# Kernel tuning notes

Measured on AMD Instinct MI355X. Metric: run time of the kernel, lower is better.

Reference implementation:

```python
import jax, jax.numpy as jnp
import numpy as np

DIM = 128    # dim (LSTM hidden size)
P = 8        # pooling_size (maxout pool width)
K = 2        # number of experts
STEPS = 4    # max_decoding_steps
M = 4096     # document length


def setup_inputs() -> dict:
    d, p, k, m = DIM, P, K, M
    keys = jax.random.split(jax.random.key(0), 26)
    s = 0.05

    def rn(kk, shape):
        return jax.random.normal(kk, shape, jnp.float32) * s

    inp = {"U": jax.random.normal(keys[0], (1, m, 2 * d), jnp.float32)}
    inp["lstm_Wih"] = rn(keys[1], (4 * d, 4 * d))
    inp["lstm_Whh"] = rn(keys[2], (4 * d, d))
    inp["lstm_bih"] = rn(keys[3], (4 * d,))
    inp["lstm_bhh"] = rn(keys[4], (4 * d,))
    i = 5
    for suf in ("s", "e"):
        inp[f"Wr_{suf}"] = rn(keys[i], (d, 5 * d)); i += 1
        inp[f"br_{suf}"] = rn(keys[i], (d,)); i += 1
        inp[f"Wg_{suf}"] = rn(keys[i], (k, 5 * d)); i += 1
        inp[f"bg_{suf}"] = rn(keys[i], (k,)); i += 1
        inp[f"We_{suf}"] = rn(keys[i], (k, p * d, 3 * d)); i += 1
        inp[f"be_{suf}"] = rn(keys[i], (k, p * d)); i += 1
        inp[f"W2_{suf}"] = rn(keys[i], (p * d, d)); i += 1
        inp[f"b2_{suf}"] = rn(keys[i], (p * d,)); i += 1
        inp[f"W3_{suf}"] = rn(keys[i], (p, 2 * d)); i += 1
        inp[f"b3_{suf}"] = rn(keys[i], (p,)); i += 1
    return inp


def _forward(U, lstm_Wih, lstm_Whh, lstm_bih, lstm_bhh,
             Wr_s, br_s, Wg_s, bg_s, We_s, be_s, W2_s, b2_s, W3_s, b3_s,
             Wr_e, br_e, Wg_e, bg_e, We_e, be_e, W2_e, b2_e, W3_e, b3_e):
    d, p = DIM, P
    Useq = U[0]                      # (m, 2d)
    m = Useq.shape[0]

    def lstm_step(x, h, c):
        g = lstm_Wih @ x + lstm_Whh @ h + lstm_bih + lstm_bhh
        i, f, gg, o = jnp.split(g, 4)  # torch LSTM gate order: i, f, g, o
        c2 = jax.nn.sigmoid(f) * c + jax.nn.sigmoid(i) * jnp.tanh(gg)
        return jax.nn.sigmoid(o) * jnp.tanh(c2), c2

    def experts(h, us, ue, Wr, br, Wg, bg, We, be):
        ctx = jnp.concatenate([h, us, ue])                 # (5d,)
        r = jnp.tanh(Wr @ ctx + br)                        # (d,)
        gate = jax.nn.softmax(Wg @ ctx + bg)               # (k,)
        inp = jnp.concatenate([Useq, jnp.broadcast_to(r, (m, d))], axis=-1)  # (m, 3d)
        z = jnp.einsum('mf,kef->kme', inp, We) + be[:, None, :]              # (k, m, p*d)
        z = z.reshape(K, m, p, d).max(axis=2)              # maxout -> (k, m, d)
        return jnp.einsum('k,kmd->md', gate, z)            # mixture -> (m, d)

    def hmn(m1, W2, b2, W3, b3):
        m2 = (m1 @ W2.T + b2).reshape(m, p, d).max(axis=1)                    # (m, d)
        return (jnp.concatenate([m1, m2], axis=-1) @ W3.T + b3).max(axis=-1)  # (m,)

    h = jnp.zeros((d,), U.dtype)
    c = jnp.zeros((d,), U.dtype)
    si = jnp.array(0, jnp.int32)
    ei = jnp.array(m - 1, jnp.int32)
    starts, ends = [], []
    for _ in range(STEPS):
        us = jnp.take(Useq, si, axis=0)
        ue = jnp.take(Useq, ei, axis=0)
        h, c = lstm_step(jnp.concatenate([us, ue]), h, c)
        ls = hmn(experts(h, us, ue, Wr_s, br_s, Wg_s, bg_s, We_s, be_s), W2_s, b2_s, W3_s, b3_s)
        le = hmn(experts(h, us, ue, Wr_e, br_e, Wg_e, bg_e, We_e, be_e), W2_e, b2_e, W3_e, b3_e)
        si = jnp.argmax(ls).astype(jnp.int32)
        ei = jnp.argmax(le).astype(jnp.int32)
        starts.append(ls)
        ends.append(le)
    # torch.cat of (1,1,m) along dim=-2 -> (1, STEPS, m)
    return jnp.stack(starts)[None], jnp.stack(ends)[None]


def reference(U, lstm_Wih, lstm_Whh, lstm_bih, lstm_bhh,
              Wr_s, br_s, Wg_s, bg_s, We_s, be_s, W2_s, b2_s, W3_s, b3_s,
              Wr_e, br_e, Wg_e, bg_e, We_e, be_e, W2_e, b2_e, W3_e, b3_e):
    return _forward(U, lstm_Wih, lstm_Whh, lstm_bih, lstm_bhh,
                    Wr_s, br_s, Wg_s, bg_s, We_s, be_s, W2_s, b2_s, W3_s, b3_s,
                    Wr_e, br_e, Wg_e, bg_e, We_e, be_e, W2_e, b2_e, W3_e, b3_e)
```

## Files before the change

### kernel.cpp

```cpp
#include <hip/hip_runtime.h>
#include <math.h>

#define DD   128
#define MM   4096
#define NSTEP 4
#define NEG_INF (-3.4e38f)

#define WS_H0   0
#define WS_C0   256
#define WS_G    512
#define WS_RS   1024
#define WS_RE   1152
#define WS_GS   1280
#define WS_SIEI 1284
#define WS_RT   2048
#define WS_Z0   8192
#define WS_W2S  (8192 + 16777216)
#define WS_USP  (WS_W2S + 262144)
#define WS_WESP (WS_USP + 1048576)
#define WS_END2 (WS_W2S + 262144)
#define WS_END4 (WS_WESP + 1048576)
#define W2SPLIT_N 262144
#define USPLIT_N  1048576
#define WESPLIT_N 1048576

typedef __attribute__((ext_vector_type(8))) short bf16x8;
typedef __attribute__((ext_vector_type(4))) float f32x4;
typedef __attribute__((ext_vector_type(4))) unsigned short u16x4;

static __device__ __forceinline__ unsigned short f2b(float x) {
  unsigned u = __float_as_uint(x);
  unsigned r = (u + 0x7fffu + ((u >> 16) & 1u)) >> 16;
  return (unsigned short)r;
}
static __device__ __forceinline__ float b2f(unsigned short h) {
  return __uint_as_float(((unsigned)h) << 16);
}
static __device__ __forceinline__ void split4(float4 v, u16x4* h, u16x4* l) {
  unsigned short h0 = f2b(v.x), h1 = f2b(v.y), h2 = f2b(v.z), h3 = f2b(v.w);
  u16x4 hh = {h0, h1, h2, h3};
  u16x4 ll = {f2b(v.x - b2f(h0)), f2b(v.y - b2f(h1)),
              f2b(v.z - b2f(h2)), f2b(v.w - b2f(h3))};
  *h = hh; *l = ll;
}
static __device__ __forceinline__ float sigm(float x) {
  return 1.f / (1.f + expf(-x));
}

__global__ void k_init(float* __restrict__ ws) {
  int t = threadIdx.x;
  if (t < 128) { ws[WS_H0 + t] = 0.f; ws[WS_C0 + t] = 0.f; }
}

__global__ void k_prep(const float* __restrict__ W2_s,
                       const float* __restrict__ W2_e,
                       const float* __restrict__ U,
                       const float* __restrict__ We_s, const float* __restrict__ We_e,
                       int do4, float* __restrict__ ws) {
  unsigned short* w2h = (unsigned short*)(ws + WS_W2S);
  unsigned short* w2l = w2h + W2SPLIT_N;
  unsigned short* uh = (unsigned short*)(ws + WS_USP);
  unsigned short* ul = uh + USPLIT_N;
  unsigned short* wh = (unsigned short*)(ws + WS_WESP);
  unsigned short* wl = wh + WESPLIT_N;
  int total = do4 ? (W2SPLIT_N + USPLIT_N + WESPLIT_N) : W2SPLIT_N;
  for (int i = blockIdx.x * blockDim.x + threadIdx.x; i < total;
       i += gridDim.x * blockDim.x) {
    if (i < W2SPLIT_N) {
      int suf = i >> 17;
      int rem = i & 131071;
      float v = (suf ? W2_e : W2_s)[rem];
      unsigned short h = f2b(v);
      w2h[i] = h; w2l[i] = f2b(v - b2f(h));
    } else if (i < W2SPLIT_N + USPLIT_N) {
      int j = i - W2SPLIT_N;
      float v = U[j];
      unsigned short h = f2b(v);
      uh[j] = h; ul[j] = f2b(v - b2f(h));
    } else {
      int j = i - W2SPLIT_N - USPLIT_N;
      int z = j >> 18;
      int rem = j & 262143;
      int e = rem >> 8, f = rem & 255;
      int suf = z >> 1, k = z & 1;
      const float* We = suf ? We_e : We_s;
      float v = We[((size_t)k * 1024 + e) * 384 + f];
      unsigned short h = f2b(v);
      wh[j] = h; wl[j] = f2b(v - b2f(h));
    }
  }
}

__global__ __launch_bounds__(256) void k_z0m2(float* __restrict__ ws) {
  __shared__ unsigned short Ah[128][40];
  __shared__ unsigned short Al[128][40];
  __shared__ unsigned short Bh[128][40];
  __shared__ unsigned short Bl[128][40];
  float* z0 = ws + WS_Z0;
  const unsigned short* uh = (const unsigned short*)(ws + WS_USP);
  const unsigned short* ul = uh + USPLIT_N;
  const unsigned short* wh = (const unsigned short*)(ws + WS_WESP);
  const unsigned short* wl = wh + WESPLIT_N;

  int t = threadIdx.x;
  int lane = t & 63, wid = t >> 6;
  int wm = wid >> 1, wn = wid & 1;
  int lr = lane & 15, lk = (lane >> 4) * 8, lq = lane >> 4;
  int m0 = blockIdx.x * 128, e0 = blockIdx.y * 128;
  int z = blockIdx.z;
  const unsigned short* bh0 = wh + (size_t)z * 262144;
  const unsigned short* bl0 = wl + (size_t)z * 262144;

  f32x4 acc[4][4];
  f32x4 zz = {0.f, 0.f, 0.f, 0.f};
#pragma unroll
  for (int i = 0; i < 4; ++i)
#pragma unroll
    for (int n = 0; n < 4; ++n) acc[i][n] = zz;

  for (int kc = 0; kc < 8; ++kc) {
    int k0 = kc * 32;
    __syncthreads();
#pragma unroll
    for (int it = 0; it < 2; ++it) {
      int idx = t + it * 256;
      int row = idx >> 2, q8 = (idx & 3) * 8;
      size_t goff = (size_t)(m0 + row) * 256 + k0 + q8;
      *(uint4*)&Ah[row][q8] = *(const uint4*)&uh[goff];
      *(uint4*)&Al[row][q8] = *(const uint4*)&ul[goff];
      size_t boff = (size_t)(e0 + row) * 256 + k0 + q8;
      *(uint4*)&Bh[row][q8] = *(const uint4*)&bh0[boff];
      *(uint4*)&Bl[row][q8] = *(const uint4*)&bl0[boff];
    }
    __syncthreads();
    bf16x8 ah[4], al[4], bh[4], bl[4];
#pragma unroll
    for (int i = 0; i < 4; ++i) {
      ah[i] = *(bf16x8*)&Ah[wm * 64 + i * 16 + lr][lk];
      al[i] = *(bf16x8*)&Al[wm * 64 + i * 16 + lr][lk];
    }
#pragma unroll
    for (int n = 0; n < 4; ++n) {
      bh[n] = *(bf16x8*)&Bh[wn * 64 + n * 16 + lr][lk];
      bl[n] = *(bf16x8*)&Bl[wn * 64 + n * 16 + lr][lk];
    }
#pragma unroll
    for (int i = 0; i < 4; ++i)
#pragma unroll
      for (int n = 0; n < 4; ++n) {
        acc[i][n] = __builtin_amdgcn_mfma_f32_16x16x32_bf16(ah[i], bh[n], acc[i][n], 0, 0, 0);
        acc[i][n] = __builtin_amdgcn_mfma_f32_16x16x32_bf16(ah[i], bl[n], acc[i][n], 0, 0, 0);
        acc[i][n] = __builtin_amdgcn_mfma_f32_16x16x32_bf16(al[i], bh[n], acc[i][n], 0, 0, 0);
      }
  }

  float* C = z0 + (size_t)z * MM * 1024;
#pragma unroll
  for (int i = 0; i < 4; ++i)
#pragma unroll
    for (int n = 0; n < 4; ++n)
#pragma unroll
      for (int r = 0; r < 4; ++r) {
        int row = m0 + wm * 64 + i * 16 + lq * 4 + r;
        int col = e0 + wn * 64 + n * 16 + lr;
        C[(size_t)row * 1024 + col] = acc[i][n][r];
      }
}

__global__ __launch_bounds__(256) void k_z0m(
    const float* __restrict__ U,
    const float* __restrict__ We_s, const float* __restrict__ We_e,
    float* __restrict__ ws) {
  __shared__ unsigned short Ah[128][40];
  __shared__ unsigned short Al[128][40];
  __shared__ unsigned short Bh[128][40];
  __shared__ unsigned short Bl[128][40];
  float* z0 = ws + WS_Z0;

  int t = threadIdx.x;
  int lane = t & 63, wid = t >> 6;
  int wm = wid >> 1, wn = wid & 1;
  int lr = lane & 15, lk = (lane >> 4) * 8, lq = lane >> 4;
  int m0 = blockIdx.x * 128, e0 = blockIdx.y * 128;
  int z = blockIdx.z;
  int suf = z >> 1, k = z & 1;
  const float* Wep = (suf ? We_e : We_s) + (size_t)k * 1024 * 384;

  f32x4 acc[4][4];
  f32x4 zz = {0.f, 0.f, 0.f, 0.f};
#pragma unroll
  for (int i = 0; i < 4; ++i)
#pragma unroll
    for (int n = 0; n < 4; ++n) acc[i][n] = zz;

  for (int kc = 0; kc < 8; ++kc) {
    int k0 = kc * 32;
    __syncthreads();
#pragma unroll
    for (int it = 0; it < 4; ++it) {
      int idx = t + it * 256;
      int row = idx >> 3, q = idx & 7;
      float4 va = *(const float4*)&U[(size_t)(m0 + row) * 256 + k0 + q * 4];
      u16x4 h, l; split4(va, &h, &l);
      *(u16x4*)&Ah[row][q * 4] = h;
      *(u16x4*)&Al[row][q * 4] = l;
      float4 vb = *(const float4*)&Wep[(size_t)(e0 + row) * 384 + k0 + q * 4];
      split4(vb, &h, &l);
      *(u16x4*)&Bh[row][q * 4] = h;
      *(u16x4*)&Bl[row][q * 4] = l;
    }
    __syncthreads();
    bf16x8 ah[4], al[4], bh[4], bl[4];
#pragma unroll
    for (int i = 0; i < 4; ++i) {
      ah[i] = *(bf16x8*)&Ah[wm * 64 + i * 16 + lr][lk];
      al[i] = *(bf16x8*)&Al[wm * 64 + i * 16 + lr][lk];
    }
#pragma unroll
    for (int n = 0; n < 4; ++n) {
      bh[n] = *(bf16x8*)&Bh[wn * 64 + n * 16 + lr][lk];
      bl[n] = *(bf16x8*)&Bl[wn * 64 + n * 16 + lr][lk];
    }
#pragma unroll
    for (int i = 0; i < 4; ++i)
#pragma unroll
      for (int n = 0; n < 4; ++n) {
        acc[i][n] = __builtin_amdgcn_mfma_f32_16x16x32_bf16(ah[i], bh[n], acc[i][n], 0, 0, 0);
        acc[i][n] = __builtin_amdgcn_mfma_f32_16x16x32_bf16(ah[i], bl[n], acc[i][n], 0, 0, 0);
        acc[i][n] = __builtin_amdgcn_mfma_f32_16x16x32_bf16(al[i], bh[n], acc[i][n], 0, 0, 0);
      }
  }

  float* C = z0 + (size_t)z * MM * 1024;
#pragma unroll
  for (int i = 0; i < 4; ++i)
#pragma unroll
    for (int n = 0; n < 4; ++n)
#pragma unroll
      for (int r = 0; r < 4; ++r) {
        int row = m0 + wm * 64 + i * 16 + lq * 4 + r;
        int col = e0 + wn * 64 + n * 16 + lr;
        C[(size_t)row * 1024 + col] = acc[i][n][r];
      }
}

__global__ __launch_bounds__(256) void k_gates(
    const float* __restrict__ U,
    const float* __restrict__ Wih, const float* __restrict__ Whh,
    const float* __restrict__ bih, const float* __restrict__ bhh,
    const float* __restrict__ out, int step,
    float* __restrict__ ws) {
  __shared__ float ctx2[640];
  __shared__ float rv[256];
  __shared__ int   ri[256];
  __shared__ int   sei[2];
  int t = threadIdx.x;
  int b = blockIdx.x;

  if (step > 0) {
    int half = t >> 7, l = t & 127;
    const float* arr = out + (size_t)half * (NSTEP * MM) + (size_t)(step - 1) * MM;
    float bv = NEG_INF; int bi = 0;
    for (int i = l; i < MM; i += 128) {
      float v = arr[i];
      if (v > bv) { bv = v; bi = i; }
    }
    rv[t] = bv; ri[t] = bi;
    __syncthreads();
    for (int s = 64; s > 0; s >>= 1) {
      if (l < s) {
        float v2 = rv[t + s]; int i2 = ri[t + s];
        if (v2 > rv[t] || (v2 == rv[t] && i2 < ri[t])) { rv[t] = v2; ri[t] = i2; }
      }
      __syncthreads();
    }
    if (l == 0) sei[half] = ri[t];
    __syncthreads();
  } else {
    if (t == 0) { sei[0] = 0; sei[1] = MM - 1; }
    __syncthreads();
  }
  int si = sei[0], ei = sei[1];
  if (b == 0 && t == 0) { ((int*)ws)[WS_SIEI] = si; ((int*)ws)[WS_SIEI + 1] = ei; }

  ctx2[t]       = U[(size_t)si * 256 + t];
  ctx2[256 + t] = U[(size_t)ei * 256 + t];
  if (t < 128) ctx2[512 + t] = ws[WS_H0 + (step & 1) * 128 + t];
  __syncthreads();

  int row = b * 16 + (t >> 4), sub = t & 15;
  const float* wih = Wih + (size_t)row * 512;
  const float* whh = Whh + (size_t)row * 128;
  float acc = 0.f;
  int e0 = sub * 40;
#pragma unroll
  for (int e = e0; e < e0 + 40; e += 4) {
    float4 w = (e < 512) ? *(const float4*)&wih[e] : *(const float4*)&whh[e - 512];
    acc += w.x * ctx2[e] + w.y * ctx2[e + 1] + w.z * ctx2[e + 2] + w.w * ctx2[e + 3];
  }
#pragma unroll
  for (int off = 8; off > 0; off >>= 1) acc += __shfl_down(acc, off, 16);
  if (sub == 0) ws[WS_G + row] = acc + bih[row] + bhh[row];
}

__global__ __launch_bounds__(256) void k_r(
    const float* __restrict__ U,
    const float* __restrict__ Wr_s, const float* __restrict__ br_s,
    const float* __restrict__ Wg_s, const float* __restrict__ bg_s,
    const float* __restrict__ Wr_e, const float* __restrict__ br_e,
    const float* __restrict__ Wg_e, const float* __restrict__ bg_e,
    int step, float* __restrict__ ws) {
  __shared__ float ctxR[640];
  __shared__ float gl[512];
  __shared__ float logit[4];
  int t = threadIdx.x, b = blockIdx.x;
  int si = ((const int*)ws)[WS_SIEI], ei = ((const int*)ws)[WS_SIEI + 1];

  gl[t] = ws[WS_G + t];
  gl[256 + t] = ws[WS_G + 256 + t];
  ctxR[128 + t] = U[(size_t)si * 256 + t];
  ctxR[384 + t] = U[(size_t)ei * 256 + t];
  __syncthreads();
  if (t < 128) {
    float ig = sigm(gl[t]);
    float fg = sigm(gl[128 + t]);
    float gg = tanhf(gl[256 + t]);
    float og = sigm(gl[384 + t]);
    float cp = ws[WS_C0 + (step & 1) * 128 + t];
    float c2 = fg * cp + ig * gg;
    float h2 = og * tanhf(c2);
    ctxR[t] = h2;
    if (b == 16) {
      ws[WS_C0 + ((step + 1) & 1) * 128 + t] = c2;
      ws[WS_H0 + ((step + 1) & 1) * 128 + t] = h2;
    }
  }
  __syncthreads();

  if (b < 16) {
    int rr = b * 16 + (t >> 4), sub = t & 15;
    int suf = rr >> 7, i = rr & 127;
    const float* Wr = suf ? Wr_e : Wr_s;
    const float* br = suf ? br_e : br_s;
    const float* w = Wr + (size_t)i * 640;
    float acc = 0.f;
    int e0 = sub * 40;
#pragma unroll
    for (int e = e0; e < e0 + 40; e += 4) {
      float4 wv = *(const float4*)&w[e];
      acc += wv.x * ctxR[e] + wv.y * ctxR[e + 1] + wv.z * ctxR[e + 2] + wv.w * ctxR[e + 3];
    }
#pragma unroll
    for (int off = 8; off > 0; off >>= 1) acc += __shfl_down(acc, off, 16);
    if (sub == 0) ws[(suf ? WS_RE : WS_RS) + i] = tanhf(acc + br[i]);
  } else {
    if (t < 64) {
      int which = t >> 4, sub = t & 15;
      const float* Wg = (which < 2) ? Wg_s : Wg_e;
      const float* bg = (which < 2) ? bg_s : bg_e;
      int i = which & 1;
      const float* w = Wg + (size_t)i * 640;
      float acc = 0.f;
      int e0 = sub * 40;
#pragma unroll
      for (int e = e0; e < e0 + 40; e += 4) {
        float4 wv = *(const float4*)&w[e];
        acc += wv.x * ctxR[e] + wv.y * ctxR[e + 1] + wv.z * ctxR[e + 2] + wv.w * ctxR[e + 3];
      }
#pragma unroll
      for (int off = 8; off > 0; off >>= 1) acc += __shfl_down(acc, off, 16);
      if (sub == 0) logit[which] = acc + bg[i];
    }
    __syncthreads();
    if (t == 0) {
      float a = logit[0], bb = logit[1], mx = fmaxf(a, bb);
      float ea = expf(a - mx), eb = expf(bb - mx), s = ea + eb;
      ws[WS_GS + 0] = ea / s; ws[WS_GS + 1] = eb / s;
      a = logit[2]; bb = logit[3]; mx = fmaxf(a, bb);
      ea = expf(a - mx); eb = expf(bb - mx); s = ea + eb;
      ws[WS_GS + 2] = ea / s; ws[WS_GS + 3] = eb / s;
    }
  }
}

__global__ __launch_bounds__(256) void k_rt(
    const float* __restrict__ We_s, const float* __restrict__ be_s,
    const float* __restrict__ We_e, const float* __restrict__ be_e,
    float* __restrict__ ws) {
  __shared__ float rsh[256];
  int t = threadIdx.x, b = blockIdx.x;
  rsh[t] = ws[WS_RS + t];
  __syncthreads();
  int lrw = t >> 2, sub = t & 3;
  int row = b * 64 + lrw;
  int suf = row >> 11, ke = row & 2047;
  const float* We = suf ? We_e : We_s;
  const float* be = suf ? be_e : be_s;
  const float* w = We + (size_t)ke * 384 + 256;
  const float* r = rsh + suf * 128;
  float acc = 0.f;
  int e0 = sub * 32;
#pragma unroll
  for (int e = e0; e < e0 + 32; e += 4) {
    float4 wv = *(const float4*)&w[e];
    acc += wv.x * r[e] + wv.y * r[e + 1] + wv.z * r[e + 2] + wv.w * r[e + 3];
  }
#pragma unroll
  for (int off = 2; off > 0; off >>= 1) acc += __shfl_down(acc, off, 4);
  if (sub == 0) ws[WS_RT + row] = acc + be[ke];
}

__global__ __launch_bounds__(256) void k_score3(
    const float* __restrict__ b2_a, const float* __restrict__ W3_a, const float* __restrict__ b3_a,
    const float* __restrict__ b2_b, const float* __restrict__ W3_b, const float* __restrict__ b3_b,
    float* __restrict__ out_a, float* __restrict__ out_b,
    float* __restrict__ ws) {
  __shared__ float rtm[2048];
  __shared__ float m1f[16][132];
  __shared__ float m2f[16][132];
  __shared__ float sj[16][8];

  const float* z0 = ws + WS_Z0;
  const unsigned short* w2base = (const unsigned short*)(ws + WS_W2S);

  int t = threadIdx.x;
  int suf = blockIdx.y;
  int m0 = blockIdx.x * 16;
  const float* b2 = suf ? b2_b : b2_a;
  const float* W3 = suf ? W3_b : W3_a;
  const float* b3 = suf ? b3_b : b3_a;
  float*     outp = suf ? out_b : out_a;
  const unsigned short* w2h = w2base + (size_t)suf * 131072;
  const unsigned short* w2l = w2base + W2SPLIT_N + (size_t)suf * 131072;

  for (int l = t; l < 2048; l += 256) rtm[l] = ws[WS_RT + suf * 2048 + l];
  float g0 = ws[WS_GS + suf * 2 + 0];
  float g1 = ws[WS_GS + suf * 2 + 1];
  __syncthreads();

  {
    int row = t >> 4, c8 = (t & 15) * 8;
    const float* p0 = z0 + ((size_t)(suf * 2 + 0) * MM + m0 + row) * 1024 + c8;
    const float* p1 = z0 + ((size_t)(suf * 2 + 1) * MM + m0 + row) * 1024 + c8;
    float4 mxa0 = {NEG_INF, NEG_INF, NEG_INF, NEG_INF}, mxb0 = mxa0;
    float4 mxa1 = mxa0, mxb1 = mxa0;
#pragma unroll
    for (int pp = 0; pp < 8; ++pp) {
      float4 va0 = *(const float4*)&p0[pp * 128];
      float4 vb0 = *(const float4*)&p0[pp * 128 + 4];
      float4 ra0 = *(const float4*)&rtm[pp * 128 + c8];
      float4 rb0 = *(const float4*)&rtm[pp * 128 + c8 + 4];
      mxa0.x = fmaxf(mxa0.x, va0.x + ra0.x); mxa0.y = fmaxf(mxa0.y, va0.y + ra0.y);
      mxa0.z = fmaxf(mxa0.z, va0.z + ra0.z); mxa0.w = fmaxf(mxa0.w, va0.w + ra0.w);
      mxb0.x = fmaxf(mxb0.x, vb0.x + rb0.x); mxb0.y = fmaxf(mxb0.y, vb0.y + rb0.y);
      mxb0.z = fmaxf(mxb0.z, vb0.z + rb0.z); mxb0.w = fmaxf(mxb0.w, vb0.w + rb0.w);
      float4 va1 = *(const float4*)&p1[pp * 128];
      float4 vb1 = *(const float4*)&p1[pp * 128 + 4];
      float4 ra1 = *(const float4*)&rtm[1024 + pp * 128 + c8];
      float4 rb1 = *(const float4*)&rtm[1024 + pp * 128 + c8 + 4];
      mxa1.x = fmaxf(mxa1.x, va1.x + ra1.x); mxa1.y = fmaxf(mxa1.y, va1.y + ra1.y);
      mxa1.z = fmaxf(mxa1.z, va1.z + ra1.z); mxa1.w = fmaxf(mxa1.w, va1.w + ra1.w);
      mxb1.x = fmaxf(mxb1.x, vb1.x + rb1.x); mxb1.y = fmaxf(mxb1.y, vb1.y + rb1.y);
      mxb1.z = fmaxf(mxb1.z, vb1.z + rb1.z); mxb1.w = fmaxf(mxb1.w, vb1.w + rb1.w);
    }
    float4 o0 = {g0 * mxa0.x + g1 * mxa1.x, g0 * mxa0.y + g1 * mxa1.y,
                 g0 * mxa0.z + g1 * mxa1.z, g0 * mxa0.w + g1 * mxa1.w};
    float4 o1 = {g0 * mxb0.x + g1 * mxb1.x, g0 * mxb0.y + g1 * mxb1.y,
                 g0 * mxb0.z + g1 * mxb1.z, g0 * mxb0.w + g1 * mxb1.w};
    *(float4*)&m1f[row][c8] = o0;
    *(float4*)&m1f[row][c8 + 4] = o1;
  }
  __syncthreads();

  int lane = t & 63, wid = t >> 6;
  int wcol = wid * 32;
  int lr = lane & 15, lk = (lane >> 4) * 8, lq = lane >> 4;
  bf16x8 ah[4], al[4];
#pragma unroll
  for (int kk = 0; kk < 4; ++kk) {
    float4 x0 = *(const float4*)&m1f[lr][kk * 32 + lk];
    float4 x1 = *(const float4*)&m1f[lr][kk * 32 + lk + 4];
    u16x4 h0, l0, h1, l1;
    split4(x0, &h0, &l0); split4(x1, &h1, &l1);
    bf16x8 a, b;
#pragma unroll
    for (int j = 0; j < 4; ++j) { a[j] = (short)h0[j]; a[4 + j] = (short)h1[j]; }
#pragma unroll
    for (int j = 0; j < 4; ++j) { b[j] = (short)l0[j]; b[4 + j] = (short)l1[j]; }
    ah[kk] = a; al[kk] = b;
  }

  float m2x[2][4];
#pragma unroll
  for (int nt = 0; nt < 2; ++nt)
#pragma unroll
    for (int r = 0; r < 4; ++r) m2x[nt][r] = NEG_INF;

  for (int sp = 0; sp < 8; ++sp) {
    f32x4 zz = {0.f, 0.f, 0.f, 0.f};
    f32x4 acc[2][2] = {{zz, zz}, {zz, zz}};
#pragma unroll
    for (int kk = 0; kk < 4; ++kk)
#pragma unroll
      for (int nt = 0; nt < 2; ++nt) {
        size_t boff = (size_t)(sp * 128 + wcol + nt * 16 + lr) * 128 + kk * 32 + lk;
        bf16x8 bhf = *(const bf16x8*)&w2h[boff];
        bf16x8 blf = *(const bf16x8*)&w2l[boff];
        int par = kk & 1;
        acc[nt][par] = __builtin_amdgcn_mfma_f32_16x16x32_bf16(ah[kk], bhf, acc[nt][par], 0, 0, 0);
        acc[nt][par] = __builtin_amdgcn_mfma_f32_16x16x32_bf16(ah[kk], blf, acc[nt][par], 0, 0, 0);
        acc[nt][par] = __builtin_amdgcn_mfma_f32_16x16x32_bf16(al[kk], bhf, acc[nt][par], 0, 0, 0);
      }
#pragma unroll
    for (int nt = 0; nt < 2; ++nt) {
      float bias = b2[sp * 128 + wcol + nt * 16 + lr];
#pragma unroll
      for (int r = 0; r < 4; ++r)
        m2x[nt][r] = fmaxf(m2x[nt][r], acc[nt][0][r] + acc[nt][1][r] + bias);
    }
  }
#pragma unroll
  for (int nt = 0; nt < 2; ++nt)
#pragma unroll
    for (int r = 0; r < 4; ++r)
      m2f[lq * 4 + r][wcol + nt * 16 + lr] = m2x[nt][r];
  __syncthreads();

  if (t < 128) {
    int row = t & 15, jp = t >> 4;
    const float* w3 = W3 + jp * 256;
    float acc = b3[jp];
    for (int f = 0; f < 128; f += 4) {
      float4 w = *(const float4*)&w3[f];
      acc += w.x * m1f[row][f] + w.y * m1f[row][f + 1] + w.z * m1f[row][f + 2] + w.w * m1f[row][f + 3];
    }
    for (int f = 0; f < 128; f += 4) {
      float4 w = *(const float4*)&w3[128 + f];
      acc += w.x * m2f[row][f] + w.y * m2f[row][f + 1] + w.z * m2f[row][f + 2] + w.w * m2f[row][f + 3];
    }
    sj[row][jp] = acc;
  }
  __syncthreads();
  if (t < 16) {
    float mx = sj[t][0];
#pragma unroll
    for (int j = 1; j < 8; ++j) mx = fmaxf(mx, sj[t][j]);
    outp[m0 + t] = mx;
  }
}

__global__ void k_score_slow(
    const float* __restrict__ U,
    const float* __restrict__ We_a, const float* __restrict__ We_b,
    const float* __restrict__ W2_a, const float* __restrict__ b2_a,
    const float* __restrict__ W3_a, const float* __restrict__ b3_a,
    const float* __restrict__ W2_b, const float* __restrict__ b2_b,
    const float* __restrict__ W3_b, const float* __restrict__ b3_b,
    float* __restrict__ out_a, float* __restrict__ out_b,
    const float* __restrict__ ws) {
  __shared__ float u[256];
  __shared__ float m1s[128];
  __shared__ float m2v[1024];
  __shared__ float m2s[128];
  __shared__ float sjs[8];
  int t = threadIdx.x;
  int m = blockIdx.x;
  int suf = blockIdx.y;
  const float* We = suf ? We_b : We_a;
  const float* W2 = suf ? W2_b : W2_a;
  const float* b2 = suf ? b2_b : b2_a;
  const float* W3 = suf ? W3_b : W3_a;
  const float* b3 = suf ? b3_b : b3_a;
  float*     outp = suf ? out_b : out_a;
  float g0 = ws[WS_GS + suf * 2 + 0];
  float g1 = ws[WS_GS + suf * 2 + 1];
  const float* rt = ws + WS_RT + suf * 2048;

  u[t] = U[(size_t)m * 256 + t];
  __syncthreads();
  if (t < 128) {
    float mx[2] = {NEG_INF, NEG_INF};
    for (int k = 0; k < 2; ++k)
      for (int pp = 0; pp < 8; ++pp) {
        int e = k * 1024 + pp * 128 + t;
        const float* w = We + (size_t)e * 384;
        float acc = rt[e];
        for (int f = 0; f < 256; f += 4) {
          float4 wv = *(const float4*)&w[f];
          acc += wv.x * u[f] + wv.y * u[f + 1] + wv.z * u[f + 2] + wv.w * u[f + 3];
        }
        mx[k] = fmaxf(mx[k], acc);
      }
    m1s[t] = g0 * mx[0] + g1 * mx[1];
  }
  __syncthreads();
  for (int e = t; e < 1024; e += 256) {
    const float* w = W2 + (size_t)e * 128;
    float acc = b2[e];
    for (int f = 0; f < 128; f += 4) {
      float4 wv = *(const float4*)&w[f];
      acc += wv.x * m1s[f] + wv.y * m1s[f + 1] + wv.z * m1s[f + 2] + wv.w * m1s[f + 3];
    }
    m2v[e] = acc;
  }
  __syncthreads();
  if (t < 128) {
    float mx = NEG_INF;
    for (int pp = 0; pp < 8; ++pp) mx = fmaxf(mx, m2v[pp * 128 + t]);
    m2s[t] = mx;
  }
  __syncthreads();
  if (t < 8) {
    const float* w3 = W3 + t * 256;
    float acc = b3[t];
    for (int f = 0; f < 128; ++f) acc += w3[f] * m1s[f];
    for (int f = 0; f < 128; ++f) acc += w3[128 + f] * m2s[f];
    sjs[t] = acc;
  }
  __syncthreads();
  if (t == 0) {
    float mx = sjs[0];
    for (int j = 1; j < 8; ++j) mx = fmaxf(mx, sjs[j]);
    outp[m] = mx;
  }
}

extern "C" void kernel_launch(void* const* d_in, const int* in_sizes, int n_in,
                              void* d_out, int out_size, void* d_ws, size_t ws_size,
                              hipStream_t stream) {
  const float* U    = (const float*)d_in[0];
  const float* Wih  = (const float*)d_in[1];
  const float* Whh  = (const float*)d_in[2];
  const float* bih  = (const float*)d_in[3];
  const float* bhh  = (const float*)d_in[4];
  const float* Wr_s = (const float*)d_in[5];
  const float* br_s = (const float*)d_in[6];
  const float* Wg_s = (const float*)d_in[7];
  const float* bg_s = (const float*)d_in[8];
  const float* We_s = (const float*)d_in[9];
  const float* be_s = (const float*)d_in[10];
  const float* W2_s = (const float*)d_in[11];
  const float* b2_s = (const float*)d_in[12];
  const float* W3_s = (const float*)d_in[13];
  const float* b3_s = (const float*)d_in[14];
  const float* Wr_e = (const float*)d_in[15];
  const float* br_e = (const float*)d_in[16];
  const float* Wg_e = (const float*)d_in[17];
  const float* bg_e = (const float*)d_in[18];
  const float* We_e = (const float*)d_in[19];
  const float* be_e = (const float*)d_in[20];
  const float* W2_e = (const float*)d_in[21];
  const float* b2_e = (const float*)d_in[22];
  const float* W3_e = (const float*)d_in[23];
  const float* b3_e = (const float*)d_in[24];
  float* out = (float*)d_out;
  float* ws  = (float*)d_ws;

  int fast4 = (ws_size >= (size_t)WS_END4 * 4);
  int fast2 = (ws_size >= (size_t)WS_END2 * 4);

  k_init<<<1, 128, 0, stream>>>(ws);
  if (fast2) {
    k_prep<<<768, 256, 0, stream>>>(W2_s, W2_e, U, We_s, We_e, fast4, ws);
    if (fast4) {
      k_z0m2<<<dim3(32, 8, 4), 256, 0, stream>>>(ws);
    } else {
      k_z0m<<<dim3(32, 8, 4), 256, 0, stream>>>(U, We_s, We_e, ws);
    }
  }

  for (int step = 0; step < NSTEP; ++step) {
    k_gates<<<32, 256, 0, stream>>>(U, Wih, Whh, bih, bhh, out, step, ws);
    k_r<<<17, 256, 0, stream>>>(U, Wr_s, br_s, Wg_s, bg_s,
                                Wr_e, br_e, Wg_e, bg_e, step, ws);
    k_rt<<<64, 256, 0, stream>>>(We_s, be_s, We_e, be_e, ws);

    float* out_s = out + (size_t)step * MM;
    float* out_e = out + (size_t)NSTEP * MM + (size_t)step * MM;

    if (fast2) {
      k_score3<<<dim3(256, 2), 256, 0, stream>>>(
          b2_s, W3_s, b3_s, b2_e, W3_e, b3_e, out_s, out_e, ws);
    } else {
      k_score_slow<<<dim3(MM, 2), 256, 0, stream>>>(
          U, We_s, We_e,
          W2_s, b2_s, W3_s, b3_s,
          W2_e, b2_e, W3_e, b3_e,
          out_s, out_e, ws);
    }
  }
}
```

Baseline: 291.1 us.

## Fuse LSTM gates, r projection and rt matvec into one per-step kernel

Merges the three per-step kernels (LSTM gate matvec, r/gate projection, and r-times-We matvec) into a single 65-block kernel. Each block redundantly recomputes the argmax, the full LSTM gates and the r vectors in shared memory, then computes its own slice of rt. This removes two kernel launches and their global round trips per decoding step. In exchange, every block re-reads the LSTM and Wr weights, which multiplies L2 traffic and lengthens the serial work per block.

```diff
diff --git a/kernel.cpp b/kernel.cpp
--- a/kernel.cpp
+++ b/kernel.cpp
@@ -244,18 +244,27 @@
       }
 }
 
-__global__ __launch_bounds__(256) void k_gates(
+__global__ __launch_bounds__(256) void k_state2(
     const float* __restrict__ U,
     const float* __restrict__ Wih, const float* __restrict__ Whh,
     const float* __restrict__ bih, const float* __restrict__ bhh,
+    const float* __restrict__ Wr_s, const float* __restrict__ br_s,
+    const float* __restrict__ Wg_s, const float* __restrict__ bg_s,
+    const float* __restrict__ We_s, const float* __restrict__ be_s,
+    const float* __restrict__ Wr_e, const float* __restrict__ br_e,
+    const float* __restrict__ Wg_e, const float* __restrict__ bg_e,
+    const float* __restrict__ We_e, const float* __restrict__ be_e,
     const float* __restrict__ out, int step,
     float* __restrict__ ws) {
-  __shared__ float ctx2[640];
+  __shared__ float ctx[640];
+  __shared__ float gl[512];
+  __shared__ float ctxR[640];
+  __shared__ float rsh[256];
   __shared__ float rv[256];
   __shared__ int   ri[256];
   __shared__ int   sei[2];
-  int t = threadIdx.x;
-  int b = blockIdx.x;
+  __shared__ float logit[4];
+  int t = threadIdx.x, b = blockIdx.x;
 
   if (step > 0) {
     int half = t >> 7, l = t & 127;
@@ -281,46 +290,34 @@
     __syncthreads();
   }
   int si = sei[0], ei = sei[1];
-  if (b == 0 && t == 0) { ((int*)ws)[WS_SIEI] = si; ((int*)ws)[WS_SIEI + 1] = ei; }
-
-  ctx2[t]       = U[(size_t)si * 256 + t];
-  ctx2[256 + t] = U[(size_t)ei * 256 + t];
-  if (t < 128) ctx2[512 + t] = ws[WS_H0 + (step & 1) * 128 + t];
-  __syncthreads();
-
-  int row = b * 16 + (t >> 4), sub = t & 15;
-  const float* wih = Wih + (size_t)row * 512;
-  const float* whh = Whh + (size_t)row * 128;
-  float acc = 0.f;
-  int e0 = sub * 40;
-#pragma unroll
-  for (int e = e0; e < e0 + 40; e += 4) {
-    float4 w = (e < 512) ? *(const float4*)&wih[e] : *(const float4*)&whh[e - 512];
-    acc += w.x * ctx2[e] + w.y * ctx2[e + 1] + w.z * ctx2[e + 2] + w.w * ctx2[e + 3];
-  }
-#pragma unroll
-  for (int off = 8; off > 0; off >>= 1) acc += __shfl_down(acc, off, 16);
-  if (sub == 0) ws[WS_G + row] = acc + bih[row] + bhh[row];
-}
-
-__global__ __launch_bounds__(256) void k_r(
-    const float* __restrict__ U,
-    const float* __restrict__ Wr_s, const float* __restrict__ br_s,
-    const float* __restrict__ Wg_s, const float* __restrict__ bg_s,
-    const float* __restrict__ Wr_e, const float* __restrict__ br_e,
-    const float* __restrict__ Wg_e, const float* __restrict__ bg_e,
-    int step, float* __restrict__ ws) {
-  __shared__ float ctxR[640];
-  __shared__ float gl[512];
-  __shared__ float logit[4];
-  int t = threadIdx.x, b = blockIdx.x;
-  int si = ((const int*)ws)[WS_SIEI], ei = ((const int*)ws)[WS_SIEI + 1];
-
-  gl[t] = ws[WS_G + t];
-  gl[256 + t] = ws[WS_G + 256 + t];
-  ctxR[128 + t] = U[(size_t)si * 256 + t];
-  ctxR[384 + t] = U[(size_t)ei * 256 + t];
-  __syncthreads();
+
+  ctx[t]       = U[(size_t)si * 256 + t];
+  ctx[256 + t] = U[(size_t)ei * 256 + t];
+  if (t < 128) ctx[512 + t] = ws[WS_H0 + (step & 1) * 128 + t];
+  __syncthreads();
+  ctxR[128 + t] = ctx[t];
+  ctxR[384 + t] = ctx[256 + t];
+
+  {
+    int sub = t & 15, rq = t >> 4;
+    for (int it = 0; it < 32; ++it) {
+      int row = it * 16 + rq;
+      const float* wih = Wih + (size_t)row * 512;
+      const float* whh = Whh + (size_t)row * 128;
+      float acc = 0.f;
+      int e0 = sub * 40;
+#pragma unroll
+      for (int e = e0; e < e0 + 40; e += 4) {
+        float4 w = (e < 512) ? *(const float4*)&wih[e] : *(const float4*)&whh[e - 512];
+        acc += w.x * ctx[e] + w.y * ctx[e + 1] + w.z * ctx[e + 2] + w.w * ctx[e + 3];
+      }
+#pragma unroll
+      for (int off = 8; off > 0; off >>= 1) acc += __shfl_down(acc, off, 16);
+      if (sub == 0) gl[row] = acc + bih[row] + bhh[row];
+    }
+  }
+  __syncthreads();
+
   if (t < 128) {
     float ig = sigm(gl[t]);
     float fg = sigm(gl[128 + t]);
@@ -330,29 +327,54 @@
     float c2 = fg * cp + ig * gg;
     float h2 = og * tanhf(c2);
     ctxR[t] = h2;
-    if (b == 16) {
+    if (b == 64) {
       ws[WS_C0 + ((step + 1) & 1) * 128 + t] = c2;
       ws[WS_H0 + ((step + 1) & 1) * 128 + t] = h2;
     }
   }
   __syncthreads();
 
-  if (b < 16) {
-    int rr = b * 16 + (t >> 4), sub = t & 15;
-    int suf = rr >> 7, i = rr & 127;
-    const float* Wr = suf ? Wr_e : Wr_s;
-    const float* br = suf ? br_e : br_s;
-    const float* w = Wr + (size_t)i * 640;
-    float acc = 0.f;
-    int e0 = sub * 40;
-#pragma unroll
-    for (int e = e0; e < e0 + 40; e += 4) {
-      float4 wv = *(const float4*)&w[e];
-      acc += wv.x * ctxR[e] + wv.y * ctxR[e + 1] + wv.z * ctxR[e + 2] + wv.w * ctxR[e + 3];
-    }
-#pragma unroll
-    for (int off = 8; off > 0; off >>= 1) acc += __shfl_down(acc, off, 16);
-    if (sub == 0) ws[(suf ? WS_RE : WS_RS) + i] = tanhf(acc + br[i]);
+  if (b < 64) {
+    {
+      int sub = t & 15, rq = t >> 4;
+      for (int it = 0; it < 16; ++it) {
+        int rr = it * 16 + rq;
+        int suf = rr >> 7, i = rr & 127;
+        const float* Wr = suf ? Wr_e : Wr_s;
+        const float* br = suf ? br_e : br_s;
+        const float* w = Wr + (size_t)i * 640;
+        float acc = 0.f;
+        int e0 = sub * 40;
+#pragma unroll
+        for (int e = e0; e < e0 + 40; e += 4) {
+          float4 wv = *(const float4*)&w[e];
+          acc += wv.x * ctxR[e] + wv.y * ctxR[e + 1] + wv.z * ctxR[e + 2] + wv.w * ctxR[e + 3];
+        }
+#pragma unroll
+        for (int off = 8; off > 0; off >>= 1) acc += __shfl_down(acc, off, 16);
+        if (sub == 0) rsh[rr] = tanhf(acc + br[i]);
+      }
+    }
+    __syncthreads();
+    {
+      int lrw = t >> 2, sub = t & 3;
+      int row = b * 64 + lrw;
+      int suf = row >> 11, ke = row & 2047;
+      const float* We = suf ? We_e : We_s;
+      const float* be = suf ? be_e : be_s;
+      const float* w = We + (size_t)ke * 384 + 256;
+      const float* r = rsh + suf * 128;
+      float acc = 0.f;
+      int e0 = sub * 32;
+#pragma unroll
+      for (int e = e0; e < e0 + 32; e += 4) {
+        float4 wv = *(const float4*)&w[e];
+        acc += wv.x * r[e] + wv.y * r[e + 1] + wv.z * r[e + 2] + wv.w * r[e + 3];
+      }
+#pragma unroll
+      for (int off = 2; off > 0; off >>= 1) acc += __shfl_down(acc, off, 4);
+      if (sub == 0) ws[WS_RT + row] = acc + be[ke];
+    }
   } else {
     if (t < 64) {
       int which = t >> 4, sub = t & 15;
@@ -381,33 +403,6 @@
       ws[WS_GS + 2] = ea / s; ws[WS_GS + 3] = eb / s;
     }
   }
-}
-
-__global__ __launch_bounds__(256) void k_rt(
-    const float* __restrict__ We_s, const float* __restrict__ be_s,
-    const float* __restrict__ We_e, const float* __restrict__ be_e,
-    float* __restrict__ ws) {
-  __shared__ float rsh[256];
-  int t = threadIdx.x, b = blockIdx.x;
-  rsh[t] = ws[WS_RS + t];
-  __syncthreads();
-  int lrw = t >> 2, sub = t & 3;
-  int row = b * 64 + lrw;
-  int suf = row >> 11, ke = row & 2047;
-  const float* We = suf ? We_e : We_s;
-  const float* be = suf ? be_e : be_s;
-  const float* w = We + (size_t)ke * 384 + 256;
-  const float* r = rsh + suf * 128;
-  float acc = 0.f;
-  int e0 = sub * 32;
-#pragma unroll
-  for (int e = e0; e < e0 + 32; e += 4) {
-    float4 wv = *(const float4*)&w[e];
-    acc += wv.x * r[e] + wv.y * r[e + 1] + wv.z * r[e + 2] + wv.w * r[e + 3];
-  }
-#pragma unroll
-  for (int off = 2; off > 0; off >>= 1) acc += __shfl_down(acc, off, 4);
-  if (sub == 0) ws[WS_RT + row] = acc + be[ke];
 }
 
 __global__ __launch_bounds__(256) void k_score3(
@@ -670,10 +665,10 @@
   }
 
   for (int step = 0; step < NSTEP; ++step) {
-    k_gates<<<32, 256, 0, stream>>>(U, Wih, Whh, bih, bhh, out, step, ws);
-    k_r<<<17, 256, 0, stream>>>(U, Wr_s, br_s, Wg_s, bg_s,
-                                Wr_e, br_e, Wg_e, bg_e, step, ws);
-    k_rt<<<64, 256, 0, stream>>>(We_s, be_s, We_e, be_e, ws);
+    k_state2<<<65, 256, 0, stream>>>(U, Wih, Whh, bih, bhh,
+                                     Wr_s, br_s, Wg_s, bg_s, We_s, be_s,
+                                     Wr_e, br_e, Wg_e, bg_e, We_e, be_e,
+                                     out, step, ws);
 
     float* out_s = out + (size_t)step * MM;
     float* out_e = out + (size_t)NSTEP * MM + (size_t)step * MM;
```

Result: slower. 476.0 us (+63.5%).
